# Optimization experiments

Measured on AMD Instinct MI355X. Metric: run time of the kernel, lower is better.

Reference implementation:

```python
import jax, jax.numpy as jnp
import numpy as np

DIM = 3072
HEADS = 24
HEAD_DIM = 128
MLP_HIDDEN = 12288
SEQ = 2048
BATCH = 1
EPS = 1e-6


def setup_inputs() -> dict:
    key = jax.random.key(0)
    ks = jax.random.split(key, 12)
    s = 0.02
    return {
        "hidden_states": jax.random.normal(ks[0], (BATCH, SEQ, DIM), jnp.float32),
        "temb": jax.random.normal(ks[1], (BATCH, DIM), jnp.float32),
        "rope_cos": jax.random.uniform(ks[2], (SEQ, HEAD_DIM), jnp.float32),
        "rope_sin": jax.random.uniform(ks[3], (SEQ, HEAD_DIM), jnp.float32),
        # AdaLN-Zero single: Linear(dim -> 3*dim)
        "norm_w": jax.random.normal(ks[4], (3 * DIM, DIM), jnp.float32) * s,
        "norm_b": jnp.zeros((3 * DIM,), jnp.float32),
        # fused QKV + MLP projection: Linear(dim -> 3*dim + mlp_hidden)
        "qkv_mlp_w": jax.random.normal(ks[5], (3 * DIM + MLP_HIDDEN, DIM), jnp.float32) * s,
        "qkv_mlp_b": jnp.zeros((3 * DIM + MLP_HIDDEN,), jnp.float32),
        # proj_out: Linear(dim + mlp_hidden -> dim)
        "proj_w": jax.random.normal(ks[6], (DIM, DIM + MLP_HIDDEN), jnp.float32) * s,
        "proj_b": jnp.zeros((DIM,), jnp.float32),
        # qk RMSNorm weights (per head_dim)
        "rms_q_w": jnp.ones((HEAD_DIM,), jnp.float32),
        "rms_k_w": jnp.ones((HEAD_DIM,), jnp.float32),
    }


def _rms_norm(x, w):
    # x: [B,S,H,D], normalize over D
    var = jnp.mean(jnp.square(x), axis=-1, keepdims=True)
    return x * jax.lax.rsqrt(var + EPS) * w


def _apply_rope(x, cos, sin):
    # x: [B,S,H,D]; cos/sin: [S,D]. diffusers use_real, unbind_dim=-1 convention.
    xr = x.reshape(*x.shape[:-1], HEAD_DIM // 2, 2)
    rot = jnp.stack([-xr[..., 1], xr[..., 0]], axis=-1).reshape(x.shape)
    c = cos[None, :, None, :]
    s = sin[None, :, None, :]
    return x * c + rot * s


def reference(hidden_states, temb, rope_cos, rope_sin, norm_w, norm_b,
              qkv_mlp_w, qkv_mlp_b, proj_w, proj_b, rms_q_w, rms_k_w):
    B, S, _ = hidden_states.shape
    residual = hidden_states

    # --- AdaLayerNormZeroSingle ---
    mod = jax.nn.silu(temb) @ norm_w.T + norm_b          # [B, 3*dim]
    shift, scale, gate = jnp.split(mod, 3, axis=-1)       # each [B, dim]
    mu = jnp.mean(hidden_states, axis=-1, keepdims=True)
    var = jnp.mean(jnp.square(hidden_states - mu), axis=-1, keepdims=True)
    ln = (hidden_states - mu) * jax.lax.rsqrt(var + EPS)
    norm_h = ln * (1.0 + scale[:, None, :]) + shift[:, None, :]

    # --- fused QKV + MLP GEMM ---
    qkv_mlp = norm_h @ qkv_mlp_w.T + qkv_mlp_b             # [B,S,3*dim+mlp]
    qkv, mlp_h = jnp.split(qkv_mlp, [3 * DIM], axis=-1)
    mlp_out = jax.nn.gelu(mlp_h, approximate=True)         # tanh GELU

    q, k, v = jnp.split(qkv, 3, axis=-1)
    q = q.reshape(B, S, HEADS, HEAD_DIM)
    k = k.reshape(B, S, HEADS, HEAD_DIM)
    v = v.reshape(B, S, HEADS, HEAD_DIM)

    # qk RMSNorm + RoPE
    q = _apply_rope(_rms_norm(q, rms_q_w), rope_cos, rope_sin)
    k = _apply_rope(_rms_norm(k, rms_k_w), rope_cos, rope_sin)

    # scaled dot-product attention
    scale_f = 1.0 / np.sqrt(HEAD_DIM)
    scores = jnp.einsum("bqhd,bkhd->bhqk", q, k) * scale_f
    probs = jax.nn.softmax(scores, axis=-1)
    attn = jnp.einsum("bhqk,bkhd->bqhd", probs, v).reshape(B, S, DIM)

    # proj_out on concat(attn, gelu(mlp)) + gated residual
    cat = jnp.concatenate([attn, mlp_out], axis=-1)        # [B,S,dim+mlp]
    proj = cat @ proj_w.T + proj_b                          # [B,S,dim]
    return gate[:, None, :] * proj + residual
```

## Files before the change

kernel.cpp:

```cpp
#include <hip/hip_runtime.h>
#include <stdint.h>

typedef __bf16 bf16;
typedef __bf16 bf16x8 __attribute__((ext_vector_type(8)));
typedef __bf16 bf16x4 __attribute__((ext_vector_type(4)));
typedef float f32x4 __attribute__((ext_vector_type(4)));

#define DIM   3072
#define SEQ   2048
#define QKVW  9216
#define MLPH  12288
#define FUSED 21504
#define CATW  15360
#define HD    128
#define NH    24

__device__ __forceinline__ void gload_lds16(const void* g, void* l) {
  __builtin_amdgcn_global_load_lds((__attribute__((address_space(1))) void*)g,
                                   (__attribute__((address_space(3))) void*)l,
                                   16, 0, 0);
}

__device__ __forceinline__ float gelu_fast(float v) {
  float u = 0.7978845608028654f * (v + 0.044715f * v * v * v);
  return v / (1.f + __expf(-2.f * u));
}

__global__ __launch_bounds__(256) void k_mod_gemv(
    const float* __restrict__ temb, const float* __restrict__ nw,
    const float* __restrict__ nb, float* __restrict__ mod)
{
  int j = blockIdx.x * 4 + (threadIdx.x >> 6);
  int lane = threadIdx.x & 63;
  const float* row = nw + (size_t)j * DIM;
  float acc = 0.f;
  #pragma unroll
  for (int k0 = 0; k0 < DIM; k0 += 256) {
    int k = k0 + lane * 4;
    float4 w = *(const float4*)(row + k);
    float4 t = *(const float4*)(temb + k);
    float s0 = t.x / (1.f + __expf(-t.x));
    float s1 = t.y / (1.f + __expf(-t.y));
    float s2 = t.z / (1.f + __expf(-t.z));
    float s3 = t.w / (1.f + __expf(-t.w));
    acc += w.x * s0 + w.y * s1 + w.z * s2 + w.w * s3;
  }
  #pragma unroll
  for (int m = 32; m >= 1; m >>= 1) acc += __shfl_xor(acc, m, 64);
  if (lane == 0) mod[j] = acc + nb[j];
}

__global__ __launch_bounds__(256) void k_ln_mod(
    const float* __restrict__ hs, const float* __restrict__ mod,
    bf16* __restrict__ nh)
{
  int m = blockIdx.x;
  int t = threadIdx.x;
  const float* x = hs + (size_t)m * DIM;
  float4 v[3];
  float s = 0.f, ss = 0.f;
  #pragma unroll
  for (int i = 0; i < 3; i++) {
    v[i] = *(const float4*)(x + i * 1024 + t * 4);
    s  += v[i].x + v[i].y + v[i].z + v[i].w;
    ss += v[i].x * v[i].x + v[i].y * v[i].y + v[i].z * v[i].z + v[i].w * v[i].w;
  }
  #pragma unroll
  for (int msk = 32; msk >= 1; msk >>= 1) {
    s  += __shfl_xor(s, msk, 64);
    ss += __shfl_xor(ss, msk, 64);
  }
  __shared__ float red[8];
  int wave = t >> 6;
  if ((t & 63) == 0) { red[wave] = s; red[4 + wave] = ss; }
  __syncthreads();
  s  = red[0] + red[1] + red[2] + red[3];
  ss = red[4] + red[5] + red[6] + red[7];
  float mu  = s * (1.f / DIM);
  float var = ss * (1.f / DIM) - mu * mu;
  float rstd = rsqrtf(var + 1e-6f);
  #pragma unroll
  for (int i = 0; i < 3; i++) {
    int col = i * 1024 + t * 4;
    const float* sc = mod + DIM + col;
    const float* sh = mod + col;
    float4 vv = v[i];
    bf16x4 o;
    o[0] = (bf16)((vv.x - mu) * rstd * (1.f + sc[0]) + sh[0]);
    o[1] = (bf16)((vv.y - mu) * rstd * (1.f + sc[1]) + sh[1]);
    o[2] = (bf16)((vv.z - mu) * rstd * (1.f + sc[2]) + sh[2]);
    o[3] = (bf16)((vv.w - mu) * rstd * (1.f + sc[3]) + sh[3]);
    *(bf16x4*)(nh + (size_t)m * DIM + col) = o;
  }
}

__global__ __launch_bounds__(256) void k_cvt(
    const float* __restrict__ s, bf16* __restrict__ d, size_t n)
{
  size_t stride = (size_t)gridDim.x * 256 * 8;
  for (size_t i = ((size_t)blockIdx.x * 256 + threadIdx.x) * 8; i < n; i += stride) {
    float4 a = *(const float4*)(s + i);
    float4 b = *(const float4*)(s + i + 4);
    bf16x8 h;
    h[0] = (bf16)a.x; h[1] = (bf16)a.y; h[2] = (bf16)a.z; h[3] = (bf16)a.w;
    h[4] = (bf16)b.x; h[5] = (bf16)b.y; h[6] = (bf16)b.z; h[7] = (bf16)b.w;
    *(bf16x8*)(d + i) = h;
  }
}

#define MFMA_B16(a, b, c) __builtin_amdgcn_mfma_f32_16x16x32_bf16(a, b, c, 0, 0, 0)

template<int MODE>
__global__ __launch_bounds__(512, 2) void k_gemm8(
    const bf16* __restrict__ A, const bf16* __restrict__ B,
    const float* __restrict__ bias, int K, int ntn, int nkp,
    bf16* __restrict__ oq, bf16* __restrict__ ocat, float* __restrict__ pk)
{
  __shared__ bf16 lds[65536];
  int tid = threadIdx.x;
  int wave = tid >> 6, lane = tid & 63;
  int wm = wave >> 2, wn = wave & 3;

  int nwg = gridDim.x;
  int bid = blockIdx.x;
  int swz = (bid & 7) * (nwg >> 3) + (bid >> 3);
  int mt = swz & 7;
  int rest = swz >> 3;
  int nt = rest % ntn;
  int kc = rest / ntn;
  int m0 = mt * 256, n0 = nt * 256;
  int Kp = K / nkp;
  int kbeg = kc * Kp;
  int NT = Kp >> 6;

  const bf16* Ag = A + (size_t)m0 * K + kbeg;
  const bf16* Bg = B + (size_t)n0 * K + kbeg;

  auto stA = [&](int kt, int q) {
    int kw = kt >= NT ? kt - NT : kt;
    #pragma unroll
    for (int j = 0; j < 2; j++) {
      int c = j * 16 + q * 8 + wave;
      gload_lds16(Ag + (size_t)((c >> 1) * 16 + (lane & 15)) * K
                     + ((c & 1) * 32 + (lane >> 4) * 8) + kw * 64,
                  &lds[((kt & 1) << 15) + c * 512]);
    }
  };
  auto stB = [&](int kt, int q) {
    int kw = kt >= NT ? kt - NT : kt;
    #pragma unroll
    for (int j = 0; j < 2; j++) {
      int v = j * 8 + wave;
      int c = (v >> 2) * 8 + q * 4 + (v & 3);
      gload_lds16(Bg + (size_t)((c >> 1) * 16 + (lane & 15)) * K
                     + ((c & 1) * 32 + (lane >> 4) * 8) + kw * 64,
                  &lds[((kt & 1) << 15) + 16384 + c * 512]);
    }
  };

  f32x4 acc[8][4];
  #pragma unroll
  for (int i = 0; i < 8; i++)
    #pragma unroll
    for (int j = 0; j < 4; j++) acc[i][j] = (f32x4){0.f, 0.f, 0.f, 0.f};

  const int abase = wm * 8192;
  const int bbase = 16384 + wn * 4096;
  const int lo = lane * 8;
  bf16x8 af[8][2], bfr[4][2];

  #define RD_A(MI0, BO) \
    _Pragma("unroll") for (int mi = 0; mi < 4; mi++) \
    _Pragma("unroll") for (int ks = 0; ks < 2; ks++) \
      af[MI0 + mi][ks] = *(const bf16x8*)&lds[(BO) + abase + ((MI0 + mi) * 2 + ks) * 512 + lo];
  #define RD_B(NI0, BO) \
    _Pragma("unroll") for (int ni = 0; ni < 2; ni++) \
    _Pragma("unroll") for (int ks = 0; ks < 2; ks++) \
      bfr[NI0 + ni][ks] = *(const bf16x8*)&lds[(BO) + bbase + ((NI0 + ni) * 2 + ks) * 512 + lo];
  #define QUAD(MI0, NI0) \
    __builtin_amdgcn_s_setprio(1); \
    _Pragma("unroll") for (int ks = 0; ks < 2; ks++) \
    _Pragma("unroll") for (int mi = 0; mi < 4; mi++) \
    _Pragma("unroll") for (int ni = 0; ni < 2; ni++) \
      acc[MI0 + mi][NI0 + ni] = MFMA_B16(af[MI0 + mi][ks], bfr[NI0 + ni][ks], acc[MI0 + mi][NI0 + ni]); \
    __builtin_amdgcn_s_setprio(0);
  #define BAR()   __builtin_amdgcn_s_barrier()
  #define LGKM0() asm volatile("s_waitcnt lgkmcnt(0)" ::: "memory")
  #define LGKM8() asm volatile("s_waitcnt lgkmcnt(8)" ::: "memory")
  #define VM6()   asm volatile("s_waitcnt vmcnt(6)" ::: "memory")
  #define SB0()   __builtin_amdgcn_sched_barrier(0)

  stA(0, 0); stB(0, 0); stA(0, 1); stB(0, 1);
  stA(1, 0); stB(1, 0); stA(1, 1);
  VM6();
  BAR();

  for (int it = 0; it < NT; it += 2) {
    int ta = it, tb = it + 1;
    RD_A(0, 0) RD_B(0, 0)
    stB(tb, 1);
    LGKM8();
    BAR(); LGKM0(); SB0();
    QUAD(0, 0)
    BAR();
    RD_A(4, 0)
    stA(ta + 2, 0);
    BAR(); LGKM0(); SB0();
    QUAD(4, 0)
    BAR();
    RD_B(2, 0)
    stB(ta + 2, 0);
    BAR(); LGKM0(); SB0();
    QUAD(0, 2)
    BAR();
    stA(ta + 2, 1);
    VM6();
    BAR(); SB0();
    QUAD(4, 2)
    BAR();
    RD_A(0, 32768) RD_B(0, 32768)
    stB(ta + 2, 1);
    LGKM8();
    BAR(); LGKM0(); SB0();
    QUAD(0, 0)
    BAR();
    RD_A(4, 32768)
    stA(tb + 2, 0);
    BAR(); LGKM0(); SB0();
    QUAD(4, 0)
    BAR();
    RD_B(2, 32768)
    stB(tb + 2, 0);
    BAR(); LGKM0(); SB0();
    QUAD(0, 2)
    BAR();
    stA(tb + 2, 1);
    VM6();
    BAR(); SB0();
    QUAD(4, 2)
    BAR();
  }

  int rr = (lane >> 4) * 4, cl = lane & 15;
  int mw0 = m0 + wm * 128, nw0 = n0 + wn * 64;
  #pragma unroll
  for (int mi = 0; mi < 8; mi++) {
    #pragma unroll
    for (int ni = 0; ni < 4; ni++) {
      int n = nw0 + ni * 16 + cl;
      #pragma unroll
      for (int r = 0; r < 4; r++) {
        int m = mw0 + mi * 16 + rr + r;
        float v = acc[mi][ni][r];
        if (MODE == 0) {
          v += bias[n];
          if (n < QKVW) {
            oq[(size_t)m * QKVW + n] = (bf16)v;
          } else {
            ocat[(size_t)m * CATW + DIM + (n - QKVW)] = (bf16)gelu_fast(v);
          }
        } else {
          pk[(size_t)kc * SEQ * DIM + (size_t)m * DIM + n] = v;
        }
      }
    }
  }
  #undef RD_A
  #undef RD_B
  #undef QUAD
  #undef BAR
  #undef LGKM0
  #undef LGKM8
  #undef VM6
  #undef SB0
}

template<int MODE>
__global__ __launch_bounds__(256) void k_gemm2(
    const bf16* __restrict__ A, const float* __restrict__ Bf,
    const float* __restrict__ bias, int K, int ntn,
    bf16* __restrict__ oq, bf16* __restrict__ ocat,
    const float* __restrict__ gate, const float* __restrict__ resid,
    float* __restrict__ of)
{
  __shared__ bf16 sA[8192];
  __shared__ bf16 sB[8192];
  int nwg = gridDim.x;
  int bid = blockIdx.x;
  int swz = (bid & 7) * (nwg >> 3) + (bid >> 3);
  int mt = swz & 15, nt = swz >> 4;
  int m0 = mt * 128, n0 = nt * 128;
  int tid = threadIdx.x;
  int wave = tid >> 6, lane = tid & 63;
  int wr = wave >> 1, wc = wave & 1;

  size_t aoff[4], boff[4];
  bf16* la[4];
  bf16* lb[4];
  #pragma unroll
  for (int i = 0; i < 4; i++) {
    int c = wave * 4 + i;
    int rt = c >> 1, kt = c & 1;
    int row = rt * 16 + (lane & 15);
    int col = kt * 32 + (lane >> 4) * 8;
    aoff[i] = (size_t)(m0 + row) * K + col;
    boff[i] = (size_t)(n0 + row) * K + col;
    la[i] = sA + c * 512;
    lb[i] = sB + c * 512;
  }
  f32x4 acc[4][4];
  #pragma unroll
  for (int i = 0; i < 4; i++)
    #pragma unroll
    for (int j = 0; j < 4; j++) acc[i][j] = (f32x4){0.f, 0.f, 0.f, 0.f};

  for (int kk = 0; kk < K; kk += 64) {
    #pragma unroll
    for (int i = 0; i < 4; i++)
      gload_lds16(A + aoff[i] + kk, la[i]);
    #pragma unroll
    for (int i = 0; i < 4; i++) {
      const float* g = Bf + boff[i] + kk;
      float4 f0 = *(const float4*)g;
      float4 f1 = *(const float4*)(g + 4);
      bf16x8 h;
      h[0] = (bf16)f0.x; h[1] = (bf16)f0.y; h[2] = (bf16)f0.z; h[3] = (bf16)f0.w;
      h[4] = (bf16)f1.x; h[5] = (bf16)f1.y; h[6] = (bf16)f1.z; h[7] = (bf16)f1.w;
      *(bf16x8*)(lb[i] + lane * 8) = h;
    }
    __syncthreads();
    #pragma unroll
    for (int ks = 0; ks < 2; ks++) {
      bf16x8 af[4], bfr[4];
      #pragma unroll
      for (int mi = 0; mi < 4; mi++)
        af[mi] = *(const bf16x8*)(sA + ((wr * 4 + mi) * 2 + ks) * 512 + lane * 8);
      #pragma unroll
      for (int nj = 0; nj < 4; nj++)
        bfr[nj] = *(const bf16x8*)(sB + ((wc * 4 + nj) * 2 + ks) * 512 + lane * 8);
      #pragma unroll
      for (int mi = 0; mi < 4; mi++)
        #pragma unroll
        for (int nj = 0; nj < 4; nj++)
          acc[mi][nj] = __builtin_amdgcn_mfma_f32_16x16x32_bf16(af[mi], bfr[nj], acc[mi][nj], 0, 0, 0);
    }
    __syncthreads();
  }

  int rr = (lane >> 4) * 4;
  int cl = lane & 15;
  #pragma unroll
  for (int mi = 0; mi < 4; mi++) {
    #pragma unroll
    for (int nj = 0; nj < 4; nj++) {
      int mbase = m0 + wr * 64 + mi * 16 + rr;
      int n = n0 + wc * 64 + nj * 16 + cl;
      #pragma unroll
      for (int r = 0; r < 4; r++) {
        int m = mbase + r;
        float v = acc[mi][nj][r] + bias[n];
        if (MODE == 0) {
          if (n < QKVW) {
            oq[(size_t)m * QKVW + n] = (bf16)v;
          } else {
            ocat[(size_t)m * CATW + DIM + (n - QKVW)] = (bf16)gelu_fast(v);
          }
        } else {
          of[(size_t)m * DIM + n] = gate[n] * v + resid[(size_t)m * DIM + n];
        }
      }
    }
  }
}

__global__ __launch_bounds__(256) void k_red(
    const float* __restrict__ pk, const float* __restrict__ bias,
    const float* __restrict__ gate, const float* __restrict__ resid,
    float* __restrict__ out, int parts)
{
  int m = blockIdx.x / 3;
  int n = (blockIdx.x % 3) * 1024 + threadIdx.x * 4;
  size_t idx = (size_t)m * DIM + n;
  f32x4 s = *(const f32x4*)(pk + idx);
  for (int p = 1; p < parts; p++) {
    f32x4 q = *(const f32x4*)(pk + (size_t)p * SEQ * DIM + idx);
    #pragma unroll
    for (int i = 0; i < 4; i++) s[i] += q[i];
  }
  f32x4 b  = *(const f32x4*)(bias + n);
  f32x4 g  = *(const f32x4*)(gate + n);
  f32x4 r  = *(const f32x4*)(resid + idx);
  f32x4 o;
  #pragma unroll
  for (int i = 0; i < 4; i++) o[i] = g[i] * (s[i] + b[i]) + r[i];
  *(f32x4*)(out + idx) = o;
}

__global__ __launch_bounds__(256) void k_rmsrope(
    bf16* __restrict__ qkv, const float* __restrict__ rc, const float* __restrict__ rs,
    const float* __restrict__ qw, const float* __restrict__ kw)
{
  int srow = blockIdx.x >> 1;
  int isk  = blockIdx.x & 1;
  int off  = isk ? DIM : 0;
  const float* w = isk ? kw : qw;
  int g = threadIdx.x >> 5, gl = threadIdx.x & 31;
  int d = gl * 4;
  #pragma unroll
  for (int hh = 0; hh < 3; hh++) {
    int h = g + hh * 8;
    bf16* p = qkv + (size_t)srow * QKVW + off + h * HD + d;
    bf16x4 u = *(const bf16x4*)p;
    float x0 = (float)u[0], x1 = (float)u[1], x2 = (float)u[2], x3 = (float)u[3];
    float ssq = x0 * x0 + x1 * x1 + x2 * x2 + x3 * x3;
    #pragma unroll
    for (int msk = 16; msk >= 1; msk >>= 1) ssq += __shfl_xor(ssq, msk, 32);
    float r = rsqrtf(ssq * (1.f / HD) + 1e-6f);
    float y0 = x0 * r * w[d], y1 = x1 * r * w[d + 1];
    float y2 = x2 * r * w[d + 2], y3 = x3 * r * w[d + 3];
    const float* c = rc + srow * HD + d;
    const float* sn = rs + srow * HD + d;
    bf16x4 o;
    o[0] = (bf16)(y0 * c[0] - y1 * sn[0]);
    o[1] = (bf16)(y1 * c[1] + y0 * sn[1]);
    o[2] = (bf16)(y2 * c[2] - y3 * sn[2]);
    o[3] = (bf16)(y3 * c[3] + y2 * sn[3]);
    *(bf16x4*)p = o;
  }
}

__global__ __launch_bounds__(256) void k_attn(
    const bf16* __restrict__ qkv, bf16* __restrict__ cat)
{
  int h  = blockIdx.y;
  int q0 = blockIdx.x * 64;
  int tid = threadIdx.x, wave = tid >> 6, lane = tid & 63;
  int r16 = lane & 15, g4 = lane >> 4;
  __shared__ bf16 sK[32 * 168];
  __shared__ bf16 sVt[128 * 40];
  __shared__ bf16 sP[4][16 * 40];

  bf16x8 qf[4];
  {
    int qrow = q0 + wave * 16 + r16;
    const bf16* qp = qkv + (size_t)qrow * QKVW + h * HD + g4 * 8;
    #pragma unroll
    for (int kc = 0; kc < 4; kc++) qf[kc] = *(const bf16x8*)(qp + kc * 32);
  }
  f32x4 oacc[8];
  #pragma unroll
  for (int dc = 0; dc < 8; dc++) oacc[dc] = (f32x4){0.f, 0.f, 0.f, 0.f};
  float mrow[4] = {-1e30f, -1e30f, -1e30f, -1e30f};
  float lrow[4] = {0.f, 0.f, 0.f, 0.f};
  const float scale = 0.08838834764831845f;

  int krow = tid >> 3, c0 = (tid & 7) * 16;
  const bf16* kbase = qkv + (size_t)krow * QKVW + DIM + h * HD + c0;
  const bf16* vbase = qkv + (size_t)krow * QKVW + 2 * DIM + h * HD + c0;

  bf16x8 kr0 = *(const bf16x8*)(kbase);
  bf16x8 kr1 = *(const bf16x8*)(kbase + 8);
  bf16x8 vr0 = *(const bf16x8*)(vbase);
  bf16x8 vr1 = *(const bf16x8*)(vbase + 8);

  for (int kv0 = 0; kv0 < SEQ; kv0 += 32) {
    *(bf16x8*)&sK[krow * 168 + c0]     = kr0;
    *(bf16x8*)&sK[krow * 168 + c0 + 8] = kr1;
    #pragma unroll
    for (int i = 0; i < 8; i++) {
      sVt[(c0 + i) * 40 + krow]     = vr0[i];
      sVt[(c0 + 8 + i) * 40 + krow] = vr1[i];
    }
    __syncthreads();
    if (kv0 + 32 < SEQ) {
      const bf16* kn = kbase + (size_t)(kv0 + 32) * QKVW;
      const bf16* vn = vbase + (size_t)(kv0 + 32) * QKVW;
      kr0 = *(const bf16x8*)(kn);
      kr1 = *(const bf16x8*)(kn + 8);
      vr0 = *(const bf16x8*)(vn);
      vr1 = *(const bf16x8*)(vn + 8);
    }

    f32x4 sv[2];
    sv[0] = (f32x4){0.f, 0.f, 0.f, 0.f};
    sv[1] = (f32x4){0.f, 0.f, 0.f, 0.f};
    #pragma unroll
    for (int kc = 0; kc < 4; kc++)
      #pragma unroll
      for (int ct = 0; ct < 2; ct++) {
        bf16x8 kf = *(const bf16x8*)&sK[(ct * 16 + r16) * 168 + kc * 32 + g4 * 8];
        sv[ct] = __builtin_amdgcn_mfma_f32_16x16x32_bf16(qf[kc], kf, sv[ct], 0, 0, 0);
      }

    bf16* sPw = &sP[wave][0];
    #pragma unroll
    for (int r = 0; r < 4; r++) {
      float a0 = sv[0][r] * scale, a1 = sv[1][r] * scale;
      float mx = fmaxf(a0, a1);
      #pragma unroll
      for (int msk = 8; msk >= 1; msk >>= 1) mx = fmaxf(mx, __shfl_xor(mx, msk, 16));
      float mnew = fmaxf(mrow[r], mx);
      float so = __expf(mrow[r] - mnew);
      float p0 = __expf(a0 - mnew), p1 = __expf(a1 - mnew);
      float rsum = p0 + p1;
      #pragma unroll
      for (int msk = 8; msk >= 1; msk >>= 1) rsum += __shfl_xor(rsum, msk, 16);
      lrow[r] = lrow[r] * so + rsum;
      mrow[r] = mnew;
      #pragma unroll
      for (int dc = 0; dc < 8; dc++) oacc[dc][r] *= so;
      int prow = g4 * 4 + r;
      sPw[prow * 40 + r16]      = (bf16)p0;
      sPw[prow * 40 + 16 + r16] = (bf16)p1;
    }
    asm volatile("s_waitcnt lgkmcnt(0)" ::: "memory");
    __builtin_amdgcn_sched_barrier(0);
    bf16x8 pa = *(const bf16x8*)&sPw[r16 * 40 + g4 * 8];
    #pragma unroll
    for (int dc = 0; dc < 8; dc++) {
      bf16x8 vf = *(const bf16x8*)&sVt[(dc * 16 + r16) * 40 + g4 * 8];
      oacc[dc] = __builtin_amdgcn_mfma_f32_16x16x32_bf16(pa, vf, oacc[dc], 0, 0, 0);
    }
    __syncthreads();
  }

  #pragma unroll
  for (int dc = 0; dc < 8; dc++) {
    #pragma unroll
    for (int r = 0; r < 4; r++) {
      int qrow = q0 + wave * 16 + g4 * 4 + r;
      int col  = h * HD + dc * 16 + r16;
      cat[(size_t)qrow * CATW + col] = (bf16)(oacc[dc][r] / lrow[r]);
    }
  }
}

extern "C" void kernel_launch(void* const* d_in, const int* in_sizes, int n_in,
                              void* d_out, int out_size, void* d_ws, size_t ws_size,
                              hipStream_t stream) {
  const float* hs      = (const float*)d_in[0];
  const float* temb    = (const float*)d_in[1];
  const float* rope_c  = (const float*)d_in[2];
  const float* rope_s  = (const float*)d_in[3];
  const float* norm_w  = (const float*)d_in[4];
  const float* norm_b  = (const float*)d_in[5];
  const float* qkvml_w = (const float*)d_in[6];
  const float* qkvml_b = (const float*)d_in[7];
  const float* proj_w  = (const float*)d_in[8];
  const float* proj_b  = (const float*)d_in[9];
  const float* rms_q_w = (const float*)d_in[10];
  const float* rms_k_w = (const float*)d_in[11];
  float* out = (float*)d_out;

  char* ws = (char*)d_ws;
  size_t off = 0;
  float* mod  = (float*)(ws + off); off += 40960;
  bf16*  nh   = (bf16*)(ws + off); off += (size_t)SEQ * DIM * 2;
  bf16*  qkvb = (bf16*)(ws + off); off += (size_t)SEQ * QKVW * 2;
  bf16*  catb = (bf16*)(ws + off); off += (size_t)SEQ * CATW * 2;
  bf16*  wqb  = (bf16*)(ws + off); off += (size_t)FUSED * DIM * 2;
  bf16*  wpb  = (bf16*)(ws + off); off += (size_t)DIM * CATW * 2;
  float* pkbf = (float*)(ws + off);
  size_t base = off;
  int parts = (ws_size >= base + (size_t)2 * SEQ * DIM * 4) ? 2 : 0;
  bool full = (ws_size >= base) && (parts > 0);

  if (full) {
    k_cvt<<<dim3(2048), dim3(256), 0, stream>>>(qkvml_w, wqb, (size_t)FUSED * DIM);
    k_cvt<<<dim3(2048), dim3(256), 0, stream>>>(proj_w, wpb, (size_t)DIM * CATW);
  }
  k_mod_gemv<<<dim3(QKVW / 4), dim3(256), 0, stream>>>(temb, norm_w, norm_b, mod);
  k_ln_mod<<<dim3(SEQ), dim3(256), 0, stream>>>(hs, mod, nh);

  if (full) {
    k_gemm8<0><<<dim3(8 * (FUSED / 256)), dim3(512), 0, stream>>>(
        nh, wqb, qkvml_b, DIM, FUSED / 256, 1, qkvb, catb, nullptr);
  } else {
    k_gemm2<0><<<dim3(16 * (FUSED / 128)), dim3(256), 0, stream>>>(
        nh, qkvml_w, qkvml_b, DIM, FUSED / 128, qkvb, catb, nullptr, nullptr, nullptr);
  }

  k_rmsrope<<<dim3(SEQ * 2), dim3(256), 0, stream>>>(qkvb, rope_c, rope_s, rms_q_w, rms_k_w);
  k_attn<<<dim3(SEQ / 64, NH), dim3(256), 0, stream>>>(qkvb, catb);

  if (full) {
    k_gemm8<1><<<dim3(8 * (DIM / 256) * parts), dim3(512), 0, stream>>>(
        catb, wpb, nullptr, CATW, DIM / 256, parts, nullptr, nullptr, pkbf);
    k_red<<<dim3(SEQ * 3), dim3(256), 0, stream>>>(pkbf, proj_b, mod + 2 * DIM, hs, out, parts);
  } else {
    k_gemm2<1><<<dim3(16 * (DIM / 128)), dim3(256), 0, stream>>>(
        catb, proj_w, proj_b, CATW, DIM / 128, nullptr, nullptr, mod + 2 * DIM, hs, out);
  }
}
```

Before: 971.5 us.

## Widen attention KV tile to 64 and add lazy softmax rescaling

The flash-attention kernel now processes 64 keys per iteration instead of 32. This halves the number of block barriers and loop overheads and doubles the MFMA work per LDS staging round. It also adds a deferred-max trick: the running max and the rescaling of the accumulators are only updated when some lane's new max exceeds the old one by more than 8. Otherwise it skips the exp and the multiply of the 32 accumulator values per row. The cost is more registers and LDS per block, which can lower occupancy, plus a bounded risk of larger exponent values in fp32/bf16 probabilities.

```diff
diff --git a/kernel.cpp b/kernel.cpp
--- a/kernel.cpp
+++ b/kernel.cpp
@@ -436,9 +436,9 @@
   int q0 = blockIdx.x * 64;
   int tid = threadIdx.x, wave = tid >> 6, lane = tid & 63;
   int r16 = lane & 15, g4 = lane >> 4;
-  __shared__ bf16 sK[32 * 168];
-  __shared__ bf16 sVt[128 * 40];
-  __shared__ bf16 sP[4][16 * 40];
+  __shared__ bf16 sK[64 * 168];
+  __shared__ bf16 sVt[128 * 72];
+  __shared__ bf16 sP[4][16 * 72];
 
   bf16x8 qf[4];
   {
@@ -460,34 +460,46 @@
 
   bf16x8 kr0 = *(const bf16x8*)(kbase);
   bf16x8 kr1 = *(const bf16x8*)(kbase + 8);
+  bf16x8 kr2 = *(const bf16x8*)(kbase + (size_t)32 * QKVW);
+  bf16x8 kr3 = *(const bf16x8*)(kbase + (size_t)32 * QKVW + 8);
   bf16x8 vr0 = *(const bf16x8*)(vbase);
   bf16x8 vr1 = *(const bf16x8*)(vbase + 8);
-
-  for (int kv0 = 0; kv0 < SEQ; kv0 += 32) {
-    *(bf16x8*)&sK[krow * 168 + c0]     = kr0;
-    *(bf16x8*)&sK[krow * 168 + c0 + 8] = kr1;
+  bf16x8 vr2 = *(const bf16x8*)(vbase + (size_t)32 * QKVW);
+  bf16x8 vr3 = *(const bf16x8*)(vbase + (size_t)32 * QKVW + 8);
+
+  for (int kv0 = 0; kv0 < SEQ; kv0 += 64) {
+    *(bf16x8*)&sK[krow * 168 + c0]            = kr0;
+    *(bf16x8*)&sK[krow * 168 + c0 + 8]        = kr1;
+    *(bf16x8*)&sK[(krow + 32) * 168 + c0]     = kr2;
+    *(bf16x8*)&sK[(krow + 32) * 168 + c0 + 8] = kr3;
     #pragma unroll
     for (int i = 0; i < 8; i++) {
-      sVt[(c0 + i) * 40 + krow]     = vr0[i];
-      sVt[(c0 + 8 + i) * 40 + krow] = vr1[i];
+      sVt[(c0 + i) * 72 + krow]          = vr0[i];
+      sVt[(c0 + 8 + i) * 72 + krow]      = vr1[i];
+      sVt[(c0 + i) * 72 + krow + 32]     = vr2[i];
+      sVt[(c0 + 8 + i) * 72 + krow + 32] = vr3[i];
     }
     __syncthreads();
-    if (kv0 + 32 < SEQ) {
-      const bf16* kn = kbase + (size_t)(kv0 + 32) * QKVW;
-      const bf16* vn = vbase + (size_t)(kv0 + 32) * QKVW;
+    if (kv0 + 64 < SEQ) {
+      const bf16* kn = kbase + (size_t)(kv0 + 64) * QKVW;
+      const bf16* vn = vbase + (size_t)(kv0 + 64) * QKVW;
       kr0 = *(const bf16x8*)(kn);
       kr1 = *(const bf16x8*)(kn + 8);
+      kr2 = *(const bf16x8*)(kn + (size_t)32 * QKVW);
+      kr3 = *(const bf16x8*)(kn + (size_t)32 * QKVW + 8);
       vr0 = *(const bf16x8*)(vn);
       vr1 = *(const bf16x8*)(vn + 8);
-    }
-
-    f32x4 sv[2];
-    sv[0] = (f32x4){0.f, 0.f, 0.f, 0.f};
-    sv[1] = (f32x4){0.f, 0.f, 0.f, 0.f};
+      vr2 = *(const bf16x8*)(vn + (size_t)32 * QKVW);
+      vr3 = *(const bf16x8*)(vn + (size_t)32 * QKVW + 8);
+    }
+
+    f32x4 sv[4];
+    #pragma unroll
+    for (int ct = 0; ct < 4; ct++) sv[ct] = (f32x4){0.f, 0.f, 0.f, 0.f};
     #pragma unroll
     for (int kc = 0; kc < 4; kc++)
       #pragma unroll
-      for (int ct = 0; ct < 2; ct++) {
+      for (int ct = 0; ct < 4; ct++) {
         bf16x8 kf = *(const bf16x8*)&sK[(ct * 16 + r16) * 168 + kc * 32 + g4 * 8];
         sv[ct] = __builtin_amdgcn_mfma_f32_16x16x32_bf16(qf[kc], kf, sv[ct], 0, 0, 0);
       }
@@ -496,30 +508,41 @@
     #pragma unroll
     for (int r = 0; r < 4; r++) {
       float a0 = sv[0][r] * scale, a1 = sv[1][r] * scale;
-      float mx = fmaxf(a0, a1);
+      float a2 = sv[2][r] * scale, a3 = sv[3][r] * scale;
+      float mx = fmaxf(fmaxf(a0, a1), fmaxf(a2, a3));
       #pragma unroll
       for (int msk = 8; msk >= 1; msk >>= 1) mx = fmaxf(mx, __shfl_xor(mx, msk, 16));
-      float mnew = fmaxf(mrow[r], mx);
-      float so = __expf(mrow[r] - mnew);
+      bool defer = __all(mx - mrow[r] <= 8.f);
+      float mnew = defer ? mrow[r] : fmaxf(mrow[r], mx);
+      if (!defer) {
+        float so = __expf(mrow[r] - mnew);
+        lrow[r] *= so;
+        #pragma unroll
+        for (int dc = 0; dc < 8; dc++) oacc[dc][r] *= so;
+        mrow[r] = mnew;
+      }
       float p0 = __expf(a0 - mnew), p1 = __expf(a1 - mnew);
-      float rsum = p0 + p1;
+      float p2 = __expf(a2 - mnew), p3 = __expf(a3 - mnew);
+      float rsum = (p0 + p1) + (p2 + p3);
       #pragma unroll
       for (int msk = 8; msk >= 1; msk >>= 1) rsum += __shfl_xor(rsum, msk, 16);
-      lrow[r] = lrow[r] * so + rsum;
-      mrow[r] = mnew;
-      #pragma unroll
-      for (int dc = 0; dc < 8; dc++) oacc[dc][r] *= so;
+      lrow[r] += rsum;
       int prow = g4 * 4 + r;
-      sPw[prow * 40 + r16]      = (bf16)p0;
-      sPw[prow * 40 + 16 + r16] = (bf16)p1;
+      sPw[prow * 72 + r16]      = (bf16)p0;
+      sPw[prow * 72 + 16 + r16] = (bf16)p1;
+      sPw[prow * 72 + 32 + r16] = (bf16)p2;
+      sPw[prow * 72 + 48 + r16] = (bf16)p3;
     }
     asm volatile("s_waitcnt lgkmcnt(0)" ::: "memory");
     __builtin_amdgcn_sched_barrier(0);
-    bf16x8 pa = *(const bf16x8*)&sPw[r16 * 40 + g4 * 8];
+    bf16x8 pa0 = *(const bf16x8*)&sPw[r16 * 72 + g4 * 8];
+    bf16x8 pa1 = *(const bf16x8*)&sPw[r16 * 72 + 32 + g4 * 8];
     #pragma unroll
     for (int dc = 0; dc < 8; dc++) {
-      bf16x8 vf = *(const bf16x8*)&sVt[(dc * 16 + r16) * 40 + g4 * 8];
-      oacc[dc] = __builtin_amdgcn_mfma_f32_16x16x32_bf16(pa, vf, oacc[dc], 0, 0, 0);
+      bf16x8 vf0 = *(const bf16x8*)&sVt[(dc * 16 + r16) * 72 + g4 * 8];
+      bf16x8 vf1 = *(const bf16x8*)&sVt[(dc * 16 + r16) * 72 + 32 + g4 * 8];
+      oacc[dc] = __builtin_amdgcn_mfma_f32_16x16x32_bf16(pa0, vf0, oacc[dc], 0, 0, 0);
+      oacc[dc] = __builtin_amdgcn_mfma_f32_16x16x32_bf16(pa1, vf1, oacc[dc], 0, 0, 0);
     }
     __syncthreads();
   }
```

After: 977.3 us. Within noise of the previous version (+0.6%).
